# Performance work log

Measured on AMD Instinct MI355X. Metric: run time of the kernel, lower is better.

The kernel has to match this reference:

```python
import jax, jax.numpy as jnp
import numpy as np

NUM_CAPSULE = 16
DIM_CAPSULE = 32
ROUTINGS = 4
EPS = 1e-07


def squash(x, axis=-1):
    # NOTE: faithful to the source: x / sqrt(sum(x^2) + eps) (unit-norm style),
    # NOT the standard Hinton squash.
    s2 = jnp.sum(x * x, axis=axis, keepdims=True)
    return x / jnp.sqrt(s2 + EPS)


def setup_inputs() -> dict:
    key = jax.random.key(0)
    k1, k2 = jax.random.split(key)
    B, N_in, D_in = 128, 1024, 256
    x = jax.random.normal(k1, (B, N_in, D_in), dtype=jnp.float32)
    # xavier_normal over (1, D_in, NUM_CAPSULE*DIM_CAPSULE)
    fan_in, fan_out = D_in, NUM_CAPSULE * DIM_CAPSULE
    std = np.sqrt(2.0 / (fan_in + fan_out))
    W = jax.random.normal(k2, (1, D_in, NUM_CAPSULE * DIM_CAPSULE), dtype=jnp.float32) * std
    return {"x": x, "W": W}


def reference(x, W):
    B, N_in, _ = x.shape
    # u_hat: [B, N_in, num_cap*dim_cap] -> [B, num_cap, N_in, dim_cap]
    u_hat = jnp.matmul(x, W[0])
    u_hat = u_hat.reshape(B, N_in, NUM_CAPSULE, DIM_CAPSULE).transpose(0, 2, 1, 3)

    b = jnp.zeros((B, NUM_CAPSULE, N_in), dtype=u_hat.dtype)
    outputs = None
    for i in range(ROUTINGS):
        # torch permutes to softmax over the num_capsule axis; equivalent to axis=1 here
        c = jax.nn.softmax(b, axis=1)                      # [B, num_cap, N_in]
        outputs = squash(jnp.einsum('bij,bijk->bik', c, u_hat))  # [B, num_cap, dim_cap]
        if i < ROUTINGS - 1:
            b = jnp.einsum('bik,bijk->bij', outputs, u_hat)
    return outputs
```

## Files before the change

kernel.cpp:

```cpp
#include <hip/hip_runtime.h>
#include <hip/hip_bf16.h>

typedef unsigned int u32;
typedef float f32x4 __attribute__((ext_vector_type(4)));
typedef __bf16 bf16x8 __attribute__((ext_vector_type(8)));

#define BATCH 128
#define NIN   1024
#define DIN   256
#define NC    16
#define DC    32
#define NCOL  512

__device__ __forceinline__ float bflo(u32 v){ return __uint_as_float(v << 16); }
__device__ __forceinline__ float bfhi(u32 v){ return __uint_as_float(v & 0xffff0000u); }
__device__ __forceinline__ u32 bfround(u32 ua){ return (ua + 0x7fffu + ((ua >> 16) & 1u)) >> 16; }
__device__ __forceinline__ u32 pack2(float a, float b){
    return (bfround(__float_as_uint(a)) & 0xffffu) | (bfround(__float_as_uint(b)) << 16);
}
__device__ __forceinline__ bf16x8 ldfrag(const u32* p){
    return __builtin_bit_cast(bf16x8, *(const uint4*)p);
}

__global__ __launch_bounds__(128) void k_wconv(const float* __restrict__ W, u32* __restrict__ Wt){
    int n = blockIdx.x, t = threadIdx.x;
    float a = W[(size_t)(2 * t)     * NCOL + n];
    float b = W[(size_t)(2 * t + 1) * NCOL + n];
    Wt[n * 128 + t] = pack2(a, b);
}

__global__ __launch_bounds__(512, 4) void k_gemm(const float* __restrict__ x, const u32* __restrict__ Wt,
                                                 u32* __restrict__ uhat, float* __restrict__ y0){
    __shared__ __align__(16) u32 sm[16640];
    u32* xl = sm;
    const int t = threadIdx.x;
    const int jb = blockIdx.x, b = blockIdx.y;
    const int lane = t & 63, wv = t >> 6;
    const int l15 = lane & 15, q = lane >> 4;

    {
        const float4* xg = (const float4*)(x + ((size_t)b * NIN + jb * 64) * DIN);
        #pragma unroll
        for (int m = 0; m < 4; m++){
            int p = t + 512 * m;
            float4 a = xg[2 * p], c = xg[2 * p + 1];
            int j = p >> 5, wq = 4 * (p & 31);
            uint4 v;
            v.x = pack2(a.x, a.y); v.y = pack2(a.z, a.w);
            v.z = pack2(c.x, c.y); v.w = pack2(c.z, c.w);
            *(uint4*)&xl[j * 128 + ((wq + 4 * j) & 127)] = v;
        }
    }
    __syncthreads();

    f32x4 acc[4][4];
    #pragma unroll
    for (int mt = 0; mt < 4; mt++)
        #pragma unroll
        for (int nt = 0; nt < 4; nt++) acc[mt][nt] = (f32x4){0.f, 0.f, 0.f, 0.f};
    const int n0w = wv * 64;
    #pragma unroll
    for (int ks = 0; ks < 8; ks++){
        bf16x8 af[4], bfr[4];
        #pragma unroll
        for (int mt = 0; mt < 4; mt++){
            int jr = mt * 16 + l15;
            af[mt] = ldfrag(&xl[jr * 128 + ((ks * 16 + q * 4 + 4 * jr) & 127)]);
        }
        #pragma unroll
        for (int nt = 0; nt < 4; nt++)
            bfr[nt] = ldfrag(&Wt[(size_t)(n0w + nt * 16 + l15) * 128 + ks * 16 + q * 4]);
        #pragma unroll
        for (int mt = 0; mt < 4; mt++)
            #pragma unroll
            for (int nt = 0; nt < 4; nt++)
                acc[mt][nt] = __builtin_amdgcn_mfma_f32_16x16x32_bf16(af[mt], bfr[nt], acc[mt][nt], 0, 0, 0);
    }

    #pragma unroll
    for (int nt = 0; nt < 4; nt++){
        float v = 0.f;
        #pragma unroll
        for (int mt = 0; mt < 4; mt++)
            #pragma unroll
            for (int r = 0; r < 4; r++) v += acc[mt][nt][r];
        v += __shfl_xor(v, 16);
        v += __shfl_xor(v, 32);
        if (lane < 16) atomicAdd(&y0[b * NCOL + n0w + nt * 16 + lane], v);
    }

    __syncthreads();
    __hip_bfloat16* cs = (__hip_bfloat16*)sm;
    #pragma unroll
    for (int mt = 0; mt < 4; mt++)
        #pragma unroll
        for (int nt = 0; nt < 4; nt++)
            #pragma unroll
            for (int r = 0; r < 4; r++)
                cs[(mt * 16 + q * 4 + r) * 520 + n0w + nt * 16 + l15] = __float2bfloat16(acc[mt][nt][r]);
    __syncthreads();

    #pragma unroll
    for (int rep = 0; rep < 8; rep++){
        int id = t + 512 * rep;
        int k8 = id & 3, j = (id >> 2) & 63, i = id >> 8;
        uint4 v = *(uint4*)&sm[j * 260 + i * 16 + k8 * 4];
        *(uint4*)&uhat[(((size_t)b * NC + i) * NIN + jb * 64 + j) * 16 + k8 * 4] = v;
    }
}

__global__ __launch_bounds__(256) void k_route_u(const u32* __restrict__ uhat, const float* __restrict__ o,
                                                 float* __restrict__ y){
    __shared__ __align__(16) u32 ul[NC * 1028];
    __shared__ float ol[NCOL];
    __shared__ float bbc[NC * 65];
    const int jc = blockIdx.x, b = blockIdx.y, t = threadIdx.x;

    ol[t] = o[b * NCOL + t];
    ol[t + 256] = o[b * NCOL + t + 256];
    {
        const u32* ub = uhat + (((size_t)b * NC) * NIN + jc * 64) * 16;
        #pragma unroll
        for (int i = 0; i < NC; i++){
            uint4 v = *(const uint4*)&ub[(size_t)i * NIN * 16 + t * 4];
            *(uint4*)&ul[i * 1028 + t * 4] = v;
        }
    }
    __syncthreads();

    {
        int i = t >> 4;
        float o_[32];
        #pragma unroll
        for (int m = 0; m < 8; m++) *(float4*)&o_[m * 4] = *(const float4*)&ol[i * DC + m * 4];
        #pragma unroll
        for (int g = 0; g < 4; g++){
            int j = (t & 15) + 16 * g;
            float acc = 0.f;
            #pragma unroll
            for (int w4 = 0; w4 < 4; w4++){
                uint4 v = *(const uint4*)&ul[i * 1028 + j * 16 + w4 * 4];
                acc += bflo(v.x) * o_[w4*8+0] + bfhi(v.x) * o_[w4*8+1]
                     + bflo(v.y) * o_[w4*8+2] + bfhi(v.y) * o_[w4*8+3]
                     + bflo(v.z) * o_[w4*8+4] + bfhi(v.z) * o_[w4*8+5]
                     + bflo(v.w) * o_[w4*8+6] + bfhi(v.w) * o_[w4*8+7];
            }
            bbc[i * 65 + j] = acc;
        }
    }
    __syncthreads();

    if (t < 64){
        float m = -1e30f;
        #pragma unroll
        for (int i = 0; i < NC; i++) m = fmaxf(m, bbc[i * 65 + t]);
        float s = 0.f;
        #pragma unroll
        for (int i = 0; i < NC; i++){ float e = __expf(bbc[i * 65 + t] - m); bbc[i * 65 + t] = e; s += e; }
        float inv = 1.f / s;
        #pragma unroll
        for (int i = 0; i < NC; i++) bbc[i * 65 + t] *= inv;
    }
    __syncthreads();

    {
        int i = t >> 4, kp = t & 15;
        float a0 = 0.f, a1 = 0.f;
        const u32* ur = &ul[i * 1028 + kp];
        const float* cr = &bbc[i * 65];
        #pragma unroll 8
        for (int j = 0; j < 64; j++){
            float c = cr[j];
            u32 v = ur[j * 16];
            a0 += c * bflo(v);
            a1 += c * bfhi(v);
        }
        atomicAdd(&y[b * NCOL + i * DC + 2 * kp],     a0);
        atomicAdd(&y[b * NCOL + i * DC + 2 * kp + 1], a1);
    }
}

__global__ __launch_bounds__(512) void k_squash(const float* __restrict__ y, float* __restrict__ o,
                                                float* __restrict__ out, int final){
    int b = blockIdx.x, t = threadIdx.x;
    float v = y[b * NCOL + t];
    float s = v * v;
    s += __shfl_xor(s, 1); s += __shfl_xor(s, 2); s += __shfl_xor(s, 4);
    s += __shfl_xor(s, 8); s += __shfl_xor(s, 16);
    float r = v / sqrtf(s + 1e-7f);
    if (final) out[b * NCOL + t] = r;
    else       o[b * NCOL + t] = r;
}

extern "C" void kernel_launch(void* const* d_in, const int* in_sizes, int n_in,
                              void* d_out, int out_size, void* d_ws, size_t ws_size,
                              hipStream_t stream){
    const float* x = (const float*)d_in[0];
    const float* W = (const float*)d_in[1];
    float* out = (float*)d_out;
    float* f = (float*)d_ws;
    float* y    = f;
    float* o    = f + 65536;
    u32*   Wt   = (u32*)(f + 131072);
    u32*   uhat = (u32*)(f + 131072 + 65536);

    hipMemsetAsync(y, 0, NCOL * BATCH * sizeof(float), stream);
    k_wconv<<<NCOL, 128, 0, stream>>>(W, Wt);
    k_gemm<<<dim3(16, BATCH), 512, 0, stream>>>(x, Wt, uhat, y);
    k_squash<<<BATCH, 512, 0, stream>>>(y, o, out, 0);
    for (int it = 1; it < 4; it++){
        hipMemsetAsync(y, 0, NCOL * BATCH * sizeof(float), stream);
        k_route_u<<<dim3(16, BATCH), 256, 0, stream>>>(uhat, o, y);
        k_squash<<<BATCH, 512, 0, stream>>>(y, o, out, it == 3 ? 1 : 0);
    }
}
```

Measured before the change: 330.7 us.

## Store u_hat in MFMA fragment-native layout and pre-swizzle W fragments

The GEMM kernel now writes u_hat directly from MFMA accumulators in a column-major-per-block layout, removing the LDS staging transpose and two barriers and cutting shared memory use. W is pre-packed into per-lane fragment order so each B fragment is one coalesced 16-byte load. The routing kernel is rewritten for the new layout with a rotation swizzle to avoid bank conflicts, and its weighted-sum phase is reorganised so each thread computes one output column. The change also drops the occupancy hint on the GEMM launch bounds and changes global store patterns, which could alter coalescing.

```diff
diff --git a/kernel.cpp b/kernel.cpp
--- a/kernel.cpp
+++ b/kernel.cpp
@@ -22,19 +22,24 @@
     return __builtin_bit_cast(bf16x8, *(const uint4*)p);
 }
 
-__global__ __launch_bounds__(128) void k_wconv(const float* __restrict__ W, u32* __restrict__ Wt){
-    int n = blockIdx.x, t = threadIdx.x;
-    float a = W[(size_t)(2 * t)     * NCOL + n];
-    float b = W[(size_t)(2 * t + 1) * NCOL + n];
-    Wt[n * 128 + t] = pack2(a, b);
-}
-
-__global__ __launch_bounds__(512, 4) void k_gemm(const float* __restrict__ x, const u32* __restrict__ Wt,
-                                                 u32* __restrict__ uhat, float* __restrict__ y0){
-    __shared__ __align__(16) u32 sm[16640];
-    u32* xl = sm;
-    const int t = threadIdx.x;
-    const int jb = blockIdx.x, b = blockIdx.y;
+__global__ __launch_bounds__(256) void k_wconv(const float* __restrict__ W, uint4* __restrict__ Wt2){
+    int id = blockIdx.x * 256 + threadIdx.x;
+    int l = id & 63, ks = (id >> 6) & 7, ntile = id >> 9;
+    int n = ntile * 16 + (l & 15);
+    int w0 = ks * 16 + (l >> 4) * 4;
+    u32 r[4];
+    #pragma unroll
+    for (int e = 0; e < 4; e++){
+        int w = w0 + e;
+        r[e] = pack2(W[(size_t)(2 * w) * NCOL + n], W[(size_t)(2 * w + 1) * NCOL + n]);
+    }
+    Wt2[id] = make_uint4(r[0], r[1], r[2], r[3]);
+}
+
+__global__ __launch_bounds__(512) void k_gemm(const float* __restrict__ x, const uint4* __restrict__ Wt2,
+                                              u32* __restrict__ uhat, float* __restrict__ y0){
+    __shared__ __align__(16) u32 xl[64 * 128];
+    const int t = threadIdx.x, jb = blockIdx.x, b = blockIdx.y;
     const int lane = t & 63, wv = t >> 6;
     const int l15 = lane & 15, q = lane >> 4;
 
@@ -58,7 +63,6 @@
     for (int mt = 0; mt < 4; mt++)
         #pragma unroll
         for (int nt = 0; nt < 4; nt++) acc[mt][nt] = (f32x4){0.f, 0.f, 0.f, 0.f};
-    const int n0w = wv * 64;
     #pragma unroll
     for (int ks = 0; ks < 8; ks++){
         bf16x8 af[4], bfr[4];
@@ -69,7 +73,7 @@
         }
         #pragma unroll
         for (int nt = 0; nt < 4; nt++)
-            bfr[nt] = ldfrag(&Wt[(size_t)(n0w + nt * 16 + l15) * 128 + ks * 16 + q * 4]);
+            bfr[nt] = __builtin_bit_cast(bf16x8, Wt2[(size_t)(((wv * 4 + nt) * 8 + ks) * 64) + lane]);
         #pragma unroll
         for (int mt = 0; mt < 4; mt++)
             #pragma unroll
@@ -86,97 +90,90 @@
             for (int r = 0; r < 4; r++) v += acc[mt][nt][r];
         v += __shfl_xor(v, 16);
         v += __shfl_xor(v, 32);
-        if (lane < 16) atomicAdd(&y0[b * NCOL + n0w + nt * 16 + lane], v);
-    }
-
-    __syncthreads();
-    __hip_bfloat16* cs = (__hip_bfloat16*)sm;
-    #pragma unroll
-    for (int mt = 0; mt < 4; mt++)
-        #pragma unroll
-        for (int nt = 0; nt < 4; nt++)
-            #pragma unroll
-            for (int r = 0; r < 4; r++)
-                cs[(mt * 16 + q * 4 + r) * 520 + n0w + nt * 16 + l15] = __float2bfloat16(acc[mt][nt][r]);
-    __syncthreads();
-
-    #pragma unroll
-    for (int rep = 0; rep < 8; rep++){
-        int id = t + 512 * rep;
-        int k8 = id & 3, j = (id >> 2) & 63, i = id >> 8;
-        uint4 v = *(uint4*)&sm[j * 260 + i * 16 + k8 * 4];
-        *(uint4*)&uhat[(((size_t)b * NC + i) * NIN + jb * 64 + j) * 16 + k8 * 4] = v;
-    }
-}
+        if (lane < 16) atomicAdd(&y0[b * NCOL + wv * 64 + nt * 16 + lane], v);
+    }
+
+    u32* ub = uhat + (((size_t)b * NC + jb) * NCOL) * 32;
+    #pragma unroll
+    for (int nt = 0; nt < 4; nt++){
+        int n = wv * 64 + nt * 16 + l15;
+        #pragma unroll
+        for (int mt = 0; mt < 4; mt++){
+            uint2 v;
+            v.x = pack2(acc[mt][nt][0], acc[mt][nt][1]);
+            v.y = pack2(acc[mt][nt][2], acc[mt][nt][3]);
+            *(uint2*)&ub[n * 32 + mt * 8 + q * 2] = v;
+        }
+    }
+}
+
+__device__ __forceinline__ int rot8(int n){ return (n + (n >> 3)) & 7; }
 
 __global__ __launch_bounds__(256) void k_route_u(const u32* __restrict__ uhat, const float* __restrict__ o,
                                                  float* __restrict__ y){
-    __shared__ __align__(16) u32 ul[NC * 1028];
+    __shared__ __align__(16) u32 ul[NCOL * 32];
     __shared__ float ol[NCOL];
-    __shared__ float bbc[NC * 65];
+    __shared__ float bbc[NC * 68];
     const int jc = blockIdx.x, b = blockIdx.y, t = threadIdx.x;
 
     ol[t] = o[b * NCOL + t];
     ol[t + 256] = o[b * NCOL + t + 256];
     {
-        const u32* ub = uhat + (((size_t)b * NC) * NIN + jc * 64) * 16;
-        #pragma unroll
-        for (int i = 0; i < NC; i++){
-            uint4 v = *(const uint4*)&ub[(size_t)i * NIN * 16 + t * 4];
-            *(uint4*)&ul[i * 1028 + t * 4] = v;
+        const uint4* ug = (const uint4*)(uhat + ((size_t)(b * NC + jc)) * NCOL * 32);
+        #pragma unroll
+        for (int m = 0; m < 16; m++){
+            int id = t + 256 * m;
+            int n = id >> 3, jq = id & 7;
+            ((uint4*)ul)[n * 8 + ((jq + rot8(n)) & 7)] = ug[id];
         }
     }
     __syncthreads();
 
     {
-        int i = t >> 4;
+        int i = t >> 4, jq2 = t & 15;
         float o_[32];
         #pragma unroll
-        for (int m = 0; m < 8; m++) *(float4*)&o_[m * 4] = *(const float4*)&ol[i * DC + m * 4];
-        #pragma unroll
-        for (int g = 0; g < 4; g++){
-            int j = (t & 15) + 16 * g;
-            float acc = 0.f;
-            #pragma unroll
-            for (int w4 = 0; w4 < 4; w4++){
-                uint4 v = *(const uint4*)&ul[i * 1028 + j * 16 + w4 * 4];
-                acc += bflo(v.x) * o_[w4*8+0] + bfhi(v.x) * o_[w4*8+1]
-                     + bflo(v.y) * o_[w4*8+2] + bfhi(v.y) * o_[w4*8+3]
-                     + bflo(v.z) * o_[w4*8+4] + bfhi(v.z) * o_[w4*8+5]
-                     + bflo(v.w) * o_[w4*8+6] + bfhi(v.w) * o_[w4*8+7];
-            }
-            bbc[i * 65 + j] = acc;
-        }
+        for (int e = 0; e < 8; e++) *(float4*)&o_[4 * e] = *(const float4*)&ol[i * DC + 4 * e];
+        float a0 = 0.f, a1 = 0.f, a2 = 0.f, a3 = 0.f;
+        #pragma unroll
+        for (int k = 0; k < 32; k++){
+            int n = i * DC + k;
+            uint2 v = *(const uint2*)&ul[n * 32 + ((2 * jq2 + 4 * rot8(n)) & 31)];
+            float ok = o_[k];
+            a0 += ok * bflo(v.x); a1 += ok * bfhi(v.x);
+            a2 += ok * bflo(v.y); a3 += ok * bfhi(v.y);
+        }
+        *(float4*)&bbc[i * 68 + 4 * jq2] = make_float4(a0, a1, a2, a3);
     }
     __syncthreads();
 
     if (t < 64){
         float m = -1e30f;
         #pragma unroll
-        for (int i = 0; i < NC; i++) m = fmaxf(m, bbc[i * 65 + t]);
+        for (int i = 0; i < NC; i++) m = fmaxf(m, bbc[i * 68 + t]);
         float s = 0.f;
         #pragma unroll
-        for (int i = 0; i < NC; i++){ float e = __expf(bbc[i * 65 + t] - m); bbc[i * 65 + t] = e; s += e; }
+        for (int i = 0; i < NC; i++){ float e = __expf(bbc[i * 68 + t] - m); bbc[i * 68 + t] = e; s += e; }
         float inv = 1.f / s;
         #pragma unroll
-        for (int i = 0; i < NC; i++) bbc[i * 65 + t] *= inv;
-    }
-    __syncthreads();
-
-    {
-        int i = t >> 4, kp = t & 15;
-        float a0 = 0.f, a1 = 0.f;
-        const u32* ur = &ul[i * 1028 + kp];
-        const float* cr = &bbc[i * 65];
-        #pragma unroll 8
-        for (int j = 0; j < 64; j++){
-            float c = cr[j];
-            u32 v = ur[j * 16];
-            a0 += c * bflo(v);
-            a1 += c * bfhi(v);
-        }
-        atomicAdd(&y[b * NCOL + i * DC + 2 * kp],     a0);
-        atomicAdd(&y[b * NCOL + i * DC + 2 * kp + 1], a1);
+        for (int i = 0; i < NC; i++) bbc[i * 68 + t] *= inv;
+    }
+    __syncthreads();
+
+    #pragma unroll
+    for (int h = 0; h < 2; h++){
+        int n = t + 256 * h;
+        int i = n >> 5;
+        float s = 0.f;
+        #pragma unroll
+        for (int w4 = 0; w4 < 8; w4++){
+            uint4 v = *(const uint4*)&ul[n * 32 + ((4 * w4 + 4 * rot8(n)) & 31)];
+            float4 c0 = *(const float4*)&bbc[i * 68 + 8 * w4];
+            float4 c1 = *(const float4*)&bbc[i * 68 + 8 * w4 + 4];
+            s += c0.x * bflo(v.x) + c0.y * bfhi(v.x) + c0.z * bflo(v.y) + c0.w * bfhi(v.y)
+               + c1.x * bflo(v.z) + c1.y * bfhi(v.z) + c1.z * bflo(v.w) + c1.w * bfhi(v.w);
+        }
+        atomicAdd(&y[b * NCOL + n], s);
     }
 }
 
@@ -201,12 +198,12 @@
     float* f = (float*)d_ws;
     float* y    = f;
     float* o    = f + 65536;
-    u32*   Wt   = (u32*)(f + 131072);
-    u32*   uhat = (u32*)(f + 131072 + 65536);
+    uint4* Wt2  = (uint4*)(f + 131072);
+    u32*   uhat = (u32*)(f + 196608);
 
     hipMemsetAsync(y, 0, NCOL * BATCH * sizeof(float), stream);
-    k_wconv<<<NCOL, 128, 0, stream>>>(W, Wt);
-    k_gemm<<<dim3(16, BATCH), 512, 0, stream>>>(x, Wt, uhat, y);
+    k_wconv<<<64, 256, 0, stream>>>(W, Wt2);
+    k_gemm<<<dim3(16, BATCH), 512, 0, stream>>>(x, Wt2, uhat, y);
     k_squash<<<BATCH, 512, 0, stream>>>(y, o, out, 0);
     for (int it = 1; it < 4; it++){
         hipMemsetAsync(y, 0, NCOL * BATCH * sizeof(float), stream);
```

Result: faster. 321.6 us (-2.7%).
